# Performance work log

Measured on AMD Instinct MI355X. Metric: run time of the kernel, lower is better.

## Reference

```python
import jax, jax.numpy as jnp
import numpy as np

B, S, E, H = 2, 2048, 1024, 16
HD = E // H  # 64


def setup_inputs() -> dict:
    key = jax.random.key(0)
    ks = jax.random.split(key, 4)
    return {
        "x": jax.random.normal(ks[0], (B, S, E), dtype=jnp.float32),
        "w_qkv": jax.random.normal(ks[1], (3 * E, E), dtype=jnp.float32) * (1.0 / np.sqrt(E)),
        "b_qkv": jnp.zeros((3 * E,), dtype=jnp.float32),
        "w_out": jax.random.normal(ks[2], (E, E), dtype=jnp.float32) * (1.0 / np.sqrt(E)),
        "b_out": jnp.zeros((E,), dtype=jnp.float32),
        "rel_emb": jax.random.normal(ks[3], (H, S, HD), dtype=jnp.float32) * (1.0 / np.sqrt(S)),
    }


def reference(x, w_qkv, b_qkv, w_out, b_out, rel_emb):
    b, s, e = x.shape
    h, hd = H, HD
    # fused QKV projection: [b, s, 3e] -> [b, s, h, 3*hd] -> [b, h, s, 3*hd]
    qkv = (jnp.einsum("bse,fe->bsf", x, w_qkv) + b_qkv).reshape(b, s, h, 3 * hd)
    qkv = qkv.transpose(0, 2, 1, 3)
    q, k, v = jnp.split(qkv, 3, axis=-1)  # each [b, h, s, hd]

    logits = jnp.einsum("bhik,bhjk->bhij", q, k) / np.sqrt(hd)

    # relative position logits (skewing trick; as written the cat/reshape/slice
    # is shape-identity, so it reduces to a direct addition)
    rel = rel_emb[:, -s:, :]  # [h, s, hd]
    rel_logits = jnp.einsum("bhik,hjk->bhij", q, rel)  # [b, h, s, s]
    rel_logits = jnp.concatenate(
        [jnp.zeros((b, h, 1, s), dtype=rel_logits.dtype), rel_logits], axis=-2
    )
    rel_logits = rel_logits.reshape(b, h, s + 1, s)[..., 1:, :]
    logits = logits + rel_logits

    weights = jax.nn.softmax(logits, axis=-1)  # [b, h, s, s]
    av = jnp.einsum("bhij,bhjd->bhid", weights, v)  # [b, h, s, hd]
    av = av.transpose(0, 2, 1, 3).reshape(b, s, e)
    out = jnp.einsum("bse,fe->bsf", av, w_out) + b_out
    return (out, weights)
```

## Files before the change

kernel.cpp:

```cpp
#include <hip/hip_runtime.h>
#include <hip/hip_bf16.h>

#define BB 2
#define SS 2048
#define EE 1024
#define HH 16
#define HD 64

typedef __attribute__((ext_vector_type(8))) __bf16 bf16x8;
typedef __attribute__((ext_vector_type(4))) __bf16 bf16x4;
typedef __attribute__((ext_vector_type(4))) float f32x4;

__device__ __forceinline__ void split2(float x, __bf16& h, __bf16& l) {
    h = (__bf16)x;
    l = (__bf16)(x - (float)h);
}

__global__ __launch_bounds__(256) void k_split(const float* __restrict__ in,
                                               __bf16* __restrict__ hi,
                                               __bf16* __restrict__ lo, int n4)
{
    int i = blockIdx.x * 256 + threadIdx.x;
    if (i >= n4) return;
    const float4 v = *(const float4*)(in + (size_t)i * 4);
    float t[4] = {v.x, v.y, v.z, v.w};
    bf16x4 h4, l4;
#pragma unroll
    for (int e = 0; e < 4; ++e) {
        __bf16 h, l; split2(t[e], h, l);
        h4[e] = h; l4[e] = l;
    }
    *(bf16x4*)(hi + (size_t)i * 4) = h4;
    *(bf16x4*)(lo + (size_t)i * 4) = l4;
}

__global__ __launch_bounds__(256) void k_qkv(
    const __bf16* __restrict__ xhi, const __bf16* __restrict__ xlo,
    const __bf16* __restrict__ whi, const __bf16* __restrict__ wlo,
    const float* __restrict__ bqkv, const float* __restrict__ rel,
    __bf16* __restrict__ qhi_ws, __bf16* __restrict__ qlo_ws,
    __bf16* __restrict__ khi_ws, __bf16* __restrict__ klo_ws,
    __bf16* __restrict__ vt_ws)
{
    __shared__ __bf16 Ahi[128][72], Alo[128][72];
    __shared__ __bf16 Bhi[64][72],  Blo[64][72];

    const int tid = threadIdx.x;
    const int lane = tid & 63;
    const int wv = tid >> 6;
    const int m0 = blockIdx.y * 128;
    const int f0 = blockIdx.x * 64;
    const int wr = (wv >> 1) * 64, wc = (wv & 1) * 32;
    const int lr = lane & 15, lg = lane >> 4;

    f32x4 acc[4][2];
#pragma unroll
    for (int a = 0; a < 4; ++a)
#pragma unroll
        for (int b = 0; b < 2; ++b) acc[a][b] = (f32x4){0.f, 0.f, 0.f, 0.f};

    for (int kt = 0; kt < 16; ++kt) {
        const int k0 = kt * 64;
        __syncthreads();
        {
            const int c = tid & 7, r0 = tid >> 3;
#pragma unroll
            for (int i = 0; i < 4; ++i) {
                const int row = r0 + i * 32;
                const size_t g = (size_t)(m0 + row) * EE + k0 + c * 8;
                *(bf16x8*)&Ahi[row][c * 8] = *(const bf16x8*)(xhi + g);
                *(bf16x8*)&Alo[row][c * 8] = *(const bf16x8*)(xlo + g);
            }
        }
        {
            const int c = tid & 7, r0 = tid >> 3;
#pragma unroll
            for (int i = 0; i < 2; ++i) {
                const int row = r0 + i * 32;
                const size_t g = (size_t)(f0 + row) * EE + k0 + c * 8;
                *(bf16x8*)&Bhi[row][c * 8] = *(const bf16x8*)(whi + g);
                *(bf16x8*)&Blo[row][c * 8] = *(const bf16x8*)(wlo + g);
            }
        }
        __syncthreads();
#pragma unroll
        for (int ks = 0; ks < 2; ++ks) {
            const int koff = ks * 32 + lg * 8;
            bf16x8 ah[4], al[4], bh[2], bl[2];
#pragma unroll
            for (int rt = 0; rt < 4; ++rt) {
                ah[rt] = *(const bf16x8*)&Ahi[wr + rt * 16 + lr][koff];
                al[rt] = *(const bf16x8*)&Alo[wr + rt * 16 + lr][koff];
            }
#pragma unroll
            for (int ct = 0; ct < 2; ++ct) {
                bh[ct] = *(const bf16x8*)&Bhi[wc + ct * 16 + lr][koff];
                bl[ct] = *(const bf16x8*)&Blo[wc + ct * 16 + lr][koff];
            }
#pragma unroll
            for (int rt = 0; rt < 4; ++rt)
#pragma unroll
                for (int ct = 0; ct < 2; ++ct) {
                    acc[rt][ct] = __builtin_amdgcn_mfma_f32_16x16x32_bf16(ah[rt], bh[ct], acc[rt][ct], 0, 0, 0);
                    acc[rt][ct] = __builtin_amdgcn_mfma_f32_16x16x32_bf16(al[rt], bh[ct], acc[rt][ct], 0, 0, 0);
                    acc[rt][ct] = __builtin_amdgcn_mfma_f32_16x16x32_bf16(ah[rt], bl[ct], acc[rt][ct], 0, 0, 0);
                }
        }
    }

    const int blk = f0 >> 6;
    const int h = blk / 3, typ = blk % 3;
#pragma unroll
    for (int rt = 0; rt < 4; ++rt) {
        const int m = m0 + wr + rt * 16 + lg * 4;
        const int b = m >> 11, s = m & 2047;
#pragma unroll
        for (int ct = 0; ct < 2; ++ct) {
            const int d = wc + ct * 16 + lr;
            const float bq = bqkv[f0 + d];
            if (typ == 0) {
                const size_t base = ((size_t)(b * HH + h) * SS + s) * HD + d;
#pragma unroll
                for (int r = 0; r < 4; ++r) {
                    __bf16 hh, ll; split2(acc[rt][ct][r] + bq, hh, ll);
                    qhi_ws[base + (size_t)r * HD] = hh;
                    qlo_ws[base + (size_t)r * HD] = ll;
                }
            } else if (typ == 1) {
                const size_t base = ((size_t)(b * HH + h) * SS + s) * HD + d;
                const size_t rb = ((size_t)h * SS + s) * HD + d;
#pragma unroll
                for (int r = 0; r < 4; ++r) {
                    const float t = (acc[rt][ct][r] + bq) * 0.125f + rel[rb + (size_t)r * HD];
                    __bf16 hh, ll; split2(t, hh, ll);
                    khi_ws[base + (size_t)r * HD] = hh;
                    klo_ws[base + (size_t)r * HD] = ll;
                }
            } else {
                const size_t base = ((size_t)(b * HH + h) * HD + d) * SS + s;
                bf16x4 pk;
#pragma unroll
                for (int r = 0; r < 4; ++r) pk[r] = (__bf16)(acc[rt][ct][r] + bq);
                *(bf16x4*)&vt_ws[base] = pk;
            }
        }
    }
}

__global__ __launch_bounds__(512, 2) void k_attn7(
    const __bf16* __restrict__ qhi_ws, const __bf16* __restrict__ qlo_ws,
    const __bf16* __restrict__ khi_ws, const __bf16* __restrict__ klo_ws,
    const __bf16* __restrict__ vt_ws,
    float* __restrict__ wts, __bf16* __restrict__ av_ws)
{
    __shared__ __bf16 KH[64][72], KL[64][72], VTS[64][72];
    __shared__ __bf16 P[8][32][72];

    const int tid = threadIdx.x;
    const int lane = tid & 63;
    const int wv = tid >> 6;
    const int lr = lane & 15, lg = lane >> 4;

    const int wgid = (blockIdx.x & 7) * 32 + (blockIdx.x >> 3);
    const int bh = wgid >> 3;
    const int q0 = (wgid & 7) * 256 + wv * 32;
    const size_t kvb = (size_t)bh * SS * HD;

    const int srow = tid >> 3;
    const int scol = (tid & 7) * 8;

    bf16x8 qh[2][2], ql[2][2];
#pragma unroll
    for (int rg = 0; rg < 2; ++rg) {
        const size_t ro = kvb + (size_t)(q0 + rg * 16 + lr) * HD + lg * 8;
#pragma unroll
        for (int kk = 0; kk < 2; ++kk) {
            qh[rg][kk] = *(const bf16x8*)(qhi_ws + ro + kk * 32);
            ql[rg][kk] = *(const bf16x8*)(qlo_ws + ro + kk * 32);
        }
    }

    const __bf16* khp = khi_ws + kvb;
    const __bf16* klp = klo_ws + kvb;
    const __bf16* vtp = vt_ws + kvb;

    float z[2][4] = {{0.f,0.f,0.f,0.f},{0.f,0.f,0.f,0.f}};
    bf16x8 sh = *(const bf16x8*)(khp + (size_t)srow * HD + scol);
    bf16x8 sl = *(const bf16x8*)(klp + (size_t)srow * HD + scol);
    for (int jt = 0; jt < 32; ++jt) {
        __syncthreads();
        *(bf16x8*)&KH[srow][scol] = sh;
        *(bf16x8*)&KL[srow][scol] = sl;
        __syncthreads();
        if (jt + 1 < 32) {
            const size_t ro = ((size_t)(jt + 1) * 64 + srow) * HD + scol;
            sh = *(const bf16x8*)(khp + ro);
            sl = *(const bf16x8*)(klp + ro);
        }
#pragma unroll
        for (int cg = 0; cg < 4; ++cg) {
            const bf16x8 kh0 = *(const bf16x8*)&KH[cg * 16 + lr][lg * 8];
            const bf16x8 kh1 = *(const bf16x8*)&KH[cg * 16 + lr][32 + lg * 8];
            const bf16x8 kl0 = *(const bf16x8*)&KL[cg * 16 + lr][lg * 8];
            const bf16x8 kl1 = *(const bf16x8*)&KL[cg * 16 + lr][32 + lg * 8];
#pragma unroll
            for (int rg = 0; rg < 2; ++rg) {
                f32x4 u = (f32x4){0.f, 0.f, 0.f, 0.f};
                u = __builtin_amdgcn_mfma_f32_16x16x32_bf16(qh[rg][0], kh0, u, 0, 0, 0);
                u = __builtin_amdgcn_mfma_f32_16x16x32_bf16(qh[rg][1], kh1, u, 0, 0, 0);
                u = __builtin_amdgcn_mfma_f32_16x16x32_bf16(ql[rg][0], kh0, u, 0, 0, 0);
                u = __builtin_amdgcn_mfma_f32_16x16x32_bf16(ql[rg][1], kh1, u, 0, 0, 0);
                u = __builtin_amdgcn_mfma_f32_16x16x32_bf16(qh[rg][0], kl0, u, 0, 0, 0);
                u = __builtin_amdgcn_mfma_f32_16x16x32_bf16(qh[rg][1], kl1, u, 0, 0, 0);
#pragma unroll
                for (int r = 0; r < 4; ++r) z[rg][r] += __expf(u[r]);
            }
        }
    }
#pragma unroll
    for (int m = 1; m < 16; m <<= 1)
#pragma unroll
        for (int rg = 0; rg < 2; ++rg)
#pragma unroll
            for (int r = 0; r < 4; ++r) z[rg][r] += __shfl_xor(z[rg][r], m, 64);
    float rz[2][4];
#pragma unroll
    for (int rg = 0; rg < 2; ++rg)
#pragma unroll
        for (int r = 0; r < 4; ++r) rz[rg][r] = 1.0f / z[rg][r];

    f32x4 pv[2][4];
#pragma unroll
    for (int rg = 0; rg < 2; ++rg)
#pragma unroll
        for (int dg = 0; dg < 4; ++dg) pv[rg][dg] = (f32x4){0.f, 0.f, 0.f, 0.f};

    float* wbase = wts + ((size_t)bh * SS + q0) * SS;

    sh = *(const bf16x8*)(khp + (size_t)srow * HD + scol);
    sl = *(const bf16x8*)(klp + (size_t)srow * HD + scol);
    bf16x8 sv = *(const bf16x8*)(vtp + (size_t)srow * SS + scol);
    for (int jt = 0; jt < 32; ++jt) {
        const int j0 = jt * 64;
        __syncthreads();
        *(bf16x8*)&KH[srow][scol] = sh;
        *(bf16x8*)&KL[srow][scol] = sl;
        *(bf16x8*)&VTS[srow][scol] = sv;
        __syncthreads();
        if (jt + 1 < 32) {
            const size_t ro = ((size_t)(jt + 1) * 64 + srow) * HD + scol;
            sh = *(const bf16x8*)(khp + ro);
            sl = *(const bf16x8*)(klp + ro);
            sv = *(const bf16x8*)(vtp + (size_t)srow * SS + j0 + 64 + scol);
        }
#pragma unroll
        for (int cg = 0; cg < 4; ++cg) {
            const bf16x8 kh0 = *(const bf16x8*)&KH[cg * 16 + lr][lg * 8];
            const bf16x8 kh1 = *(const bf16x8*)&KH[cg * 16 + lr][32 + lg * 8];
            const bf16x8 kl0 = *(const bf16x8*)&KL[cg * 16 + lr][lg * 8];
            const bf16x8 kl1 = *(const bf16x8*)&KL[cg * 16 + lr][32 + lg * 8];
#pragma unroll
            for (int rg = 0; rg < 2; ++rg) {
                f32x4 u = (f32x4){0.f, 0.f, 0.f, 0.f};
                u = __builtin_amdgcn_mfma_f32_16x16x32_bf16(qh[rg][0], kh0, u, 0, 0, 0);
                u = __builtin_amdgcn_mfma_f32_16x16x32_bf16(qh[rg][1], kh1, u, 0, 0, 0);
                u = __builtin_amdgcn_mfma_f32_16x16x32_bf16(ql[rg][0], kh0, u, 0, 0, 0);
                u = __builtin_amdgcn_mfma_f32_16x16x32_bf16(ql[rg][1], kh1, u, 0, 0, 0);
                u = __builtin_amdgcn_mfma_f32_16x16x32_bf16(qh[rg][0], kl0, u, 0, 0, 0);
                u = __builtin_amdgcn_mfma_f32_16x16x32_bf16(qh[rg][1], kl1, u, 0, 0, 0);
#pragma unroll
                for (int r = 0; r < 4; ++r)
                    P[wv][rg * 16 + lg * 4 + r][cg * 16 + lr] =
                        (__bf16)(__expf(u[r]) * rz[rg][r]);
            }
        }
        {
            bf16x8 vb[4][2];
#pragma unroll
            for (int dg = 0; dg < 4; ++dg)
#pragma unroll
                for (int kk = 0; kk < 2; ++kk)
                    vb[dg][kk] = *(const bf16x8*)&VTS[dg * 16 + lr][kk * 32 + lg * 8];
#pragma unroll
            for (int rg = 0; rg < 2; ++rg) {
                const bf16x8 pa0 = *(const bf16x8*)&P[wv][rg * 16 + lr][lg * 8];
                const bf16x8 pa1 = *(const bf16x8*)&P[wv][rg * 16 + lr][32 + lg * 8];
#pragma unroll
                for (int dg = 0; dg < 4; ++dg) {
                    pv[rg][dg] = __builtin_amdgcn_mfma_f32_16x16x32_bf16(pa0, vb[dg][0], pv[rg][dg], 0, 0, 0);
                    pv[rg][dg] = __builtin_amdgcn_mfma_f32_16x16x32_bf16(pa1, vb[dg][1], pv[rg][dg], 0, 0, 0);
                }
            }
        }
#pragma unroll
        for (int it = 0; it < 8; ++it) {
            const int row = it * 4 + lg;
            const bf16x4 u = *(const bf16x4*)&P[wv][row][lr * 4];
            float4 o;
            o.x = (float)u[0]; o.y = (float)u[1]; o.z = (float)u[2]; o.w = (float)u[3];
            *(float4*)(wbase + (size_t)row * SS + j0 + lr * 4) = o;
        }
    }

    {
        const int b = bh >> 4, h = bh & 15;
#pragma unroll
        for (int rg = 0; rg < 2; ++rg)
#pragma unroll
            for (int dg = 0; dg < 4; ++dg)
#pragma unroll
                for (int r = 0; r < 4; ++r) {
                    const int s = q0 + rg * 16 + lg * 4 + r;
                    av_ws[((size_t)(b * SS + s)) * EE + h * HD + dg * 16 + lr] =
                        (__bf16)pv[rg][dg][r];
                }
    }
}

__global__ __launch_bounds__(256) void k_oproj(
    const __bf16* __restrict__ av_ws, const float* __restrict__ w_out,
    const float* __restrict__ b_out, float* __restrict__ out)
{
    __shared__ __bf16 Abf[128][72];
    __shared__ __bf16 Bbf[64][72];
    const int tid = threadIdx.x;
    const int lane = tid & 63;
    const int wv = tid >> 6;
    const int m0 = blockIdx.y * 128, f0 = blockIdx.x * 64;
    const int wr = (wv >> 1) * 64, wc = (wv & 1) * 32;
    const int lr = lane & 15, lg = lane >> 4;

    f32x4 acc[4][2];
#pragma unroll
    for (int a = 0; a < 4; ++a)
#pragma unroll
        for (int b = 0; b < 2; ++b) acc[a][b] = (f32x4){0.f, 0.f, 0.f, 0.f};

    for (int kt = 0; kt < 16; ++kt) {
        const int k0 = kt * 64;
        __syncthreads();
        {
            const int c = tid & 7, r0 = tid >> 3;
#pragma unroll
            for (int i = 0; i < 4; ++i) {
                const int row = r0 + i * 32;
                *(bf16x8*)&Abf[row][c * 8] =
                    *(const bf16x8*)(av_ws + (size_t)(m0 + row) * EE + k0 + c * 8);
            }
        }
        {
            const int c = tid & 15, r0 = tid >> 4;
#pragma unroll
            for (int i = 0; i < 4; ++i) {
                const int row = r0 + i * 16;
                const float4 v = *(const float4*)(w_out + (size_t)(f0 + row) * EE + k0 + c * 4);
                bf16x4 pk;
                pk[0] = (__bf16)v.x; pk[1] = (__bf16)v.y;
                pk[2] = (__bf16)v.z; pk[3] = (__bf16)v.w;
                *(bf16x4*)&Bbf[row][c * 4] = pk;
            }
        }
        __syncthreads();
#pragma unroll
        for (int ks = 0; ks < 2; ++ks) {
            const int koff = ks * 32 + lg * 8;
            bf16x8 a[4], b[2];
#pragma unroll
            for (int rt = 0; rt < 4; ++rt) a[rt] = *(const bf16x8*)&Abf[wr + rt * 16 + lr][koff];
#pragma unroll
            for (int ct = 0; ct < 2; ++ct) b[ct] = *(const bf16x8*)&Bbf[wc + ct * 16 + lr][koff];
#pragma unroll
            for (int rt = 0; rt < 4; ++rt)
#pragma unroll
                for (int ct = 0; ct < 2; ++ct)
                    acc[rt][ct] = __builtin_amdgcn_mfma_f32_16x16x32_bf16(a[rt], b[ct], acc[rt][ct], 0, 0, 0);
        }
    }
#pragma unroll
    for (int rt = 0; rt < 4; ++rt) {
        const int m = m0 + wr + rt * 16 + lg * 4;
#pragma unroll
        for (int ct = 0; ct < 2; ++ct) {
            const int f = f0 + wc + ct * 16 + lr;
            const float bo = b_out[f];
#pragma unroll
            for (int r = 0; r < 4; ++r)
                out[(size_t)(m + r) * EE + f] = acc[rt][ct][r] + bo;
        }
    }
}

extern "C" void kernel_launch(void* const* d_in, const int* in_sizes, int n_in,
                              void* d_out, int out_size, void* d_ws, size_t ws_size,
                              hipStream_t stream)
{
    const float* x    = (const float*)d_in[0];
    const float* wqkv = (const float*)d_in[1];
    const float* bqkv = (const float*)d_in[2];
    const float* wo   = (const float*)d_in[3];
    const float* bo   = (const float*)d_in[4];
    const float* rel  = (const float*)d_in[5];

    float* out = (float*)d_out;
    float* wts = out + (size_t)BB * SS * EE;

    const size_t NQ = (size_t)BB * HH * SS * HD;
    __bf16* qhi_ws = (__bf16*)d_ws;
    __bf16* qlo_ws = qhi_ws + NQ;
    __bf16* khi_ws = qlo_ws + NQ;
    __bf16* klo_ws = khi_ws + NQ;
    __bf16* vt_ws  = klo_ws + NQ;
    __bf16* av_ws  = vt_ws + NQ;

    __bf16* xhi = (__bf16*)wts;
    __bf16* xlo = xhi + (size_t)BB * SS * EE;
    __bf16* whi = xlo + (size_t)BB * SS * EE;
    __bf16* wlo = whi + (size_t)3 * EE * EE;

    k_split<<<dim3((BB * SS * EE) / 1024), 256, 0, stream>>>(x, xhi, xlo, (BB * SS * EE) / 4);
    k_split<<<dim3((3 * EE * EE) / 1024), 256, 0, stream>>>(wqkv, whi, wlo, (3 * EE * EE) / 4);
    k_qkv<<<dim3(48, 32), 256, 0, stream>>>(xhi, xlo, whi, wlo, bqkv, rel,
                                            qhi_ws, qlo_ws, khi_ws, klo_ws, vt_ws);
    k_attn7<<<dim3(256), 512, 0, stream>>>(qhi_ws, qlo_ws, khi_ws, klo_ws,
                                           vt_ws, wts, av_ws);
    k_oproj<<<dim3(EE / 64, (BB * SS) / 128), 256, 0, stream>>>(av_ws, wo, bo, out);
}
```

Measured before the change: 342.8 us.

## Fuse bf16 hi/lo split into QKV GEMM and double-buffer attention K/V tiles

```diff
diff --git a/kernel.cpp b/kernel.cpp
--- a/kernel.cpp
+++ b/kernel.cpp
@@ -16,27 +16,8 @@
     l = (__bf16)(x - (float)h);
 }
 
-__global__ __launch_bounds__(256) void k_split(const float* __restrict__ in,
-                                               __bf16* __restrict__ hi,
-                                               __bf16* __restrict__ lo, int n4)
-{
-    int i = blockIdx.x * 256 + threadIdx.x;
-    if (i >= n4) return;
-    const float4 v = *(const float4*)(in + (size_t)i * 4);
-    float t[4] = {v.x, v.y, v.z, v.w};
-    bf16x4 h4, l4;
-#pragma unroll
-    for (int e = 0; e < 4; ++e) {
-        __bf16 h, l; split2(t[e], h, l);
-        h4[e] = h; l4[e] = l;
-    }
-    *(bf16x4*)(hi + (size_t)i * 4) = h4;
-    *(bf16x4*)(lo + (size_t)i * 4) = l4;
-}
-
 __global__ __launch_bounds__(256) void k_qkv(
-    const __bf16* __restrict__ xhi, const __bf16* __restrict__ xlo,
-    const __bf16* __restrict__ whi, const __bf16* __restrict__ wlo,
+    const float* __restrict__ xx, const float* __restrict__ ww,
     const float* __restrict__ bqkv, const float* __restrict__ rel,
     __bf16* __restrict__ qhi_ws, __bf16* __restrict__ qlo_ws,
     __bf16* __restrict__ khi_ws, __bf16* __restrict__ klo_ws,
@@ -67,9 +48,18 @@
 #pragma unroll
             for (int i = 0; i < 4; ++i) {
                 const int row = r0 + i * 32;
-                const size_t g = (size_t)(m0 + row) * EE + k0 + c * 8;
-                *(bf16x8*)&Ahi[row][c * 8] = *(const bf16x8*)(xhi + g);
-                *(bf16x8*)&Alo[row][c * 8] = *(const bf16x8*)(xlo + g);
+                const float* gp = xx + (size_t)(m0 + row) * EE + k0 + c * 8;
+                const float4 v0 = *(const float4*)gp;
+                const float4 v1 = *(const float4*)(gp + 4);
+                float t[8] = {v0.x, v0.y, v0.z, v0.w, v1.x, v1.y, v1.z, v1.w};
+                bf16x8 hi, lo;
+#pragma unroll
+                for (int e = 0; e < 8; ++e) {
+                    __bf16 h, l; split2(t[e], h, l);
+                    hi[e] = h; lo[e] = l;
+                }
+                *(bf16x8*)&Ahi[row][c * 8] = hi;
+                *(bf16x8*)&Alo[row][c * 8] = lo;
             }
         }
         {
@@ -77,9 +67,18 @@
 #pragma unroll
             for (int i = 0; i < 2; ++i) {
                 const int row = r0 + i * 32;
-                const size_t g = (size_t)(f0 + row) * EE + k0 + c * 8;
-                *(bf16x8*)&Bhi[row][c * 8] = *(const bf16x8*)(whi + g);
-                *(bf16x8*)&Blo[row][c * 8] = *(const bf16x8*)(wlo + g);
+                const float* gp = ww + (size_t)(f0 + row) * EE + k0 + c * 8;
+                const float4 v0 = *(const float4*)gp;
+                const float4 v1 = *(const float4*)(gp + 4);
+                float t[8] = {v0.x, v0.y, v0.z, v0.w, v1.x, v1.y, v1.z, v1.w};
+                bf16x8 hi, lo;
+#pragma unroll
+                for (int e = 0; e < 8; ++e) {
+                    __bf16 h, l; split2(t[e], h, l);
+                    hi[e] = h; lo[e] = l;
+                }
+                *(bf16x8*)&Bhi[row][c * 8] = hi;
+                *(bf16x8*)&Blo[row][c * 8] = lo;
             }
         }
         __syncthreads();
@@ -147,13 +146,13 @@
     }
 }
 
-__global__ __launch_bounds__(512, 2) void k_attn7(
+__global__ __launch_bounds__(512, 1) void k_attn8(
     const __bf16* __restrict__ qhi_ws, const __bf16* __restrict__ qlo_ws,
     const __bf16* __restrict__ khi_ws, const __bf16* __restrict__ klo_ws,
     const __bf16* __restrict__ vt_ws,
     float* __restrict__ wts, __bf16* __restrict__ av_ws)
 {
-    __shared__ __bf16 KH[64][72], KL[64][72], VTS[64][72];
+    __shared__ __bf16 KH[2][64][72], KL[2][64][72], VTS[2][64][72];
     __shared__ __bf16 P[8][32][72];
 
     const int tid = threadIdx.x;
@@ -185,36 +184,43 @@
     const __bf16* vtp = vt_ws + kvb;
 
     float z[2][4] = {{0.f,0.f,0.f,0.f},{0.f,0.f,0.f,0.f}};
-    bf16x8 sh = *(const bf16x8*)(khp + (size_t)srow * HD + scol);
-    bf16x8 sl = *(const bf16x8*)(klp + (size_t)srow * HD + scol);
-    for (int jt = 0; jt < 32; ++jt) {
-        __syncthreads();
-        *(bf16x8*)&KH[srow][scol] = sh;
-        *(bf16x8*)&KL[srow][scol] = sl;
-        __syncthreads();
-        if (jt + 1 < 32) {
-            const size_t ro = ((size_t)(jt + 1) * 64 + srow) * HD + scol;
-            sh = *(const bf16x8*)(khp + ro);
-            sl = *(const bf16x8*)(klp + ro);
-        }
-#pragma unroll
-        for (int cg = 0; cg < 4; ++cg) {
-            const bf16x8 kh0 = *(const bf16x8*)&KH[cg * 16 + lr][lg * 8];
-            const bf16x8 kh1 = *(const bf16x8*)&KH[cg * 16 + lr][32 + lg * 8];
-            const bf16x8 kl0 = *(const bf16x8*)&KL[cg * 16 + lr][lg * 8];
-            const bf16x8 kl1 = *(const bf16x8*)&KL[cg * 16 + lr][32 + lg * 8];
-#pragma unroll
-            for (int rg = 0; rg < 2; ++rg) {
-                f32x4 u = (f32x4){0.f, 0.f, 0.f, 0.f};
-                u = __builtin_amdgcn_mfma_f32_16x16x32_bf16(qh[rg][0], kh0, u, 0, 0, 0);
-                u = __builtin_amdgcn_mfma_f32_16x16x32_bf16(qh[rg][1], kh1, u, 0, 0, 0);
-                u = __builtin_amdgcn_mfma_f32_16x16x32_bf16(ql[rg][0], kh0, u, 0, 0, 0);
-                u = __builtin_amdgcn_mfma_f32_16x16x32_bf16(ql[rg][1], kh1, u, 0, 0, 0);
-                u = __builtin_amdgcn_mfma_f32_16x16x32_bf16(qh[rg][0], kl0, u, 0, 0, 0);
-                u = __builtin_amdgcn_mfma_f32_16x16x32_bf16(qh[rg][1], kl1, u, 0, 0, 0);
-#pragma unroll
-                for (int r = 0; r < 4; ++r) z[rg][r] += __expf(u[r]);
-            }
+    {
+        bf16x8 sh = *(const bf16x8*)(khp + (size_t)srow * HD + scol);
+        bf16x8 sl = *(const bf16x8*)(klp + (size_t)srow * HD + scol);
+        *(bf16x8*)&KH[0][srow][scol] = sh;
+        *(bf16x8*)&KL[0][srow][scol] = sl;
+        __syncthreads();
+        for (int jt = 0; jt < 32; ++jt) {
+            const int cur = jt & 1;
+            if (jt + 1 < 32) {
+                const size_t ro = ((size_t)(jt + 1) * 64 + srow) * HD + scol;
+                sh = *(const bf16x8*)(khp + ro);
+                sl = *(const bf16x8*)(klp + ro);
+            }
+#pragma unroll
+            for (int cg = 0; cg < 4; ++cg) {
+                const bf16x8 kh0 = *(const bf16x8*)&KH[cur][cg * 16 + lr][lg * 8];
+                const bf16x8 kh1 = *(const bf16x8*)&KH[cur][cg * 16 + lr][32 + lg * 8];
+                const bf16x8 kl0 = *(const bf16x8*)&KL[cur][cg * 16 + lr][lg * 8];
+                const bf16x8 kl1 = *(const bf16x8*)&KL[cur][cg * 16 + lr][32 + lg * 8];
+#pragma unroll
+                for (int rg = 0; rg < 2; ++rg) {
+                    f32x4 u = (f32x4){0.f, 0.f, 0.f, 0.f};
+                    u = __builtin_amdgcn_mfma_f32_16x16x32_bf16(qh[rg][0], kh0, u, 0, 0, 0);
+                    u = __builtin_amdgcn_mfma_f32_16x16x32_bf16(qh[rg][1], kh1, u, 0, 0, 0);
+                    u = __builtin_amdgcn_mfma_f32_16x16x32_bf16(ql[rg][0], kh0, u, 0, 0, 0);
+                    u = __builtin_amdgcn_mfma_f32_16x16x32_bf16(ql[rg][1], kh1, u, 0, 0, 0);
+                    u = __builtin_amdgcn_mfma_f32_16x16x32_bf16(qh[rg][0], kl0, u, 0, 0, 0);
+                    u = __builtin_amdgcn_mfma_f32_16x16x32_bf16(qh[rg][1], kl1, u, 0, 0, 0);
+#pragma unroll
+                    for (int r = 0; r < 4; ++r) z[rg][r] += __expf(u[r]);
+                }
+            }
+            if (jt + 1 < 32) {
+                *(bf16x8*)&KH[cur ^ 1][srow][scol] = sh;
+                *(bf16x8*)&KL[cur ^ 1][srow][scol] = sl;
+            }
+            __syncthreads();
         }
     }
 #pragma unroll
@@ -237,68 +243,77 @@
 
     float* wbase = wts + ((size_t)bh * SS + q0) * SS;
 
-    sh = *(const bf16x8*)(khp + (size_t)srow * HD + scol);
-    sl = *(const bf16x8*)(klp + (size_t)srow * HD + scol);
-    bf16x8 sv = *(const bf16x8*)(vtp + (size_t)srow * SS + scol);
-    for (int jt = 0; jt < 32; ++jt) {
-        const int j0 = jt * 64;
-        __syncthreads();
-        *(bf16x8*)&KH[srow][scol] = sh;
-        *(bf16x8*)&KL[srow][scol] = sl;
-        *(bf16x8*)&VTS[srow][scol] = sv;
-        __syncthreads();
-        if (jt + 1 < 32) {
-            const size_t ro = ((size_t)(jt + 1) * 64 + srow) * HD + scol;
-            sh = *(const bf16x8*)(khp + ro);
-            sl = *(const bf16x8*)(klp + ro);
-            sv = *(const bf16x8*)(vtp + (size_t)srow * SS + j0 + 64 + scol);
-        }
-#pragma unroll
-        for (int cg = 0; cg < 4; ++cg) {
-            const bf16x8 kh0 = *(const bf16x8*)&KH[cg * 16 + lr][lg * 8];
-            const bf16x8 kh1 = *(const bf16x8*)&KH[cg * 16 + lr][32 + lg * 8];
-            const bf16x8 kl0 = *(const bf16x8*)&KL[cg * 16 + lr][lg * 8];
-            const bf16x8 kl1 = *(const bf16x8*)&KL[cg * 16 + lr][32 + lg * 8];
-#pragma unroll
-            for (int rg = 0; rg < 2; ++rg) {
-                f32x4 u = (f32x4){0.f, 0.f, 0.f, 0.f};
-                u = __builtin_amdgcn_mfma_f32_16x16x32_bf16(qh[rg][0], kh0, u, 0, 0, 0);
-                u = __builtin_amdgcn_mfma_f32_16x16x32_bf16(qh[rg][1], kh1, u, 0, 0, 0);
-                u = __builtin_amdgcn_mfma_f32_16x16x32_bf16(ql[rg][0], kh0, u, 0, 0, 0);
-                u = __builtin_amdgcn_mfma_f32_16x16x32_bf16(ql[rg][1], kh1, u, 0, 0, 0);
-                u = __builtin_amdgcn_mfma_f32_16x16x32_bf16(qh[rg][0], kl0, u, 0, 0, 0);
-                u = __builtin_amdgcn_mfma_f32_16x16x32_bf16(qh[rg][1], kl1, u, 0, 0, 0);
-#pragma unroll
-                for (int r = 0; r < 4; ++r)
-                    P[wv][rg * 16 + lg * 4 + r][cg * 16 + lr] =
-                        (__bf16)(__expf(u[r]) * rz[rg][r]);
-            }
-        }
-        {
-            bf16x8 vb[4][2];
-#pragma unroll
-            for (int dg = 0; dg < 4; ++dg)
-#pragma unroll
-                for (int kk = 0; kk < 2; ++kk)
-                    vb[dg][kk] = *(const bf16x8*)&VTS[dg * 16 + lr][kk * 32 + lg * 8];
-#pragma unroll
-            for (int rg = 0; rg < 2; ++rg) {
-                const bf16x8 pa0 = *(const bf16x8*)&P[wv][rg * 16 + lr][lg * 8];
-                const bf16x8 pa1 = *(const bf16x8*)&P[wv][rg * 16 + lr][32 + lg * 8];
-#pragma unroll
-                for (int dg = 0; dg < 4; ++dg) {
-                    pv[rg][dg] = __builtin_amdgcn_mfma_f32_16x16x32_bf16(pa0, vb[dg][0], pv[rg][dg], 0, 0, 0);
-                    pv[rg][dg] = __builtin_amdgcn_mfma_f32_16x16x32_bf16(pa1, vb[dg][1], pv[rg][dg], 0, 0, 0);
-                }
-            }
-        }
-#pragma unroll
-        for (int it = 0; it < 8; ++it) {
-            const int row = it * 4 + lg;
-            const bf16x4 u = *(const bf16x4*)&P[wv][row][lr * 4];
-            float4 o;
-            o.x = (float)u[0]; o.y = (float)u[1]; o.z = (float)u[2]; o.w = (float)u[3];
-            *(float4*)(wbase + (size_t)row * SS + j0 + lr * 4) = o;
+    {
+        bf16x8 sh = *(const bf16x8*)(khp + (size_t)srow * HD + scol);
+        bf16x8 sl = *(const bf16x8*)(klp + (size_t)srow * HD + scol);
+        bf16x8 sv = *(const bf16x8*)(vtp + (size_t)srow * SS + scol);
+        *(bf16x8*)&KH[0][srow][scol] = sh;
+        *(bf16x8*)&KL[0][srow][scol] = sl;
+        *(bf16x8*)&VTS[0][srow][scol] = sv;
+        __syncthreads();
+        for (int jt = 0; jt < 32; ++jt) {
+            const int cur = jt & 1;
+            const int j0 = jt * 64;
+            if (jt + 1 < 32) {
+                const size_t ro = ((size_t)(jt + 1) * 64 + srow) * HD + scol;
+                sh = *(const bf16x8*)(khp + ro);
+                sl = *(const bf16x8*)(klp + ro);
+                sv = *(const bf16x8*)(vtp + (size_t)srow * SS + j0 + 64 + scol);
+            }
+#pragma unroll
+            for (int cg = 0; cg < 4; ++cg) {
+                const bf16x8 kh0 = *(const bf16x8*)&KH[cur][cg * 16 + lr][lg * 8];
+                const bf16x8 kh1 = *(const bf16x8*)&KH[cur][cg * 16 + lr][32 + lg * 8];
+                const bf16x8 kl0 = *(const bf16x8*)&KL[cur][cg * 16 + lr][lg * 8];
+                const bf16x8 kl1 = *(const bf16x8*)&KL[cur][cg * 16 + lr][32 + lg * 8];
+#pragma unroll
+                for (int rg = 0; rg < 2; ++rg) {
+                    f32x4 u = (f32x4){0.f, 0.f, 0.f, 0.f};
+                    u = __builtin_amdgcn_mfma_f32_16x16x32_bf16(qh[rg][0], kh0, u, 0, 0, 0);
+                    u = __builtin_amdgcn_mfma_f32_16x16x32_bf16(qh[rg][1], kh1, u, 0, 0, 0);
+                    u = __builtin_amdgcn_mfma_f32_16x16x32_bf16(ql[rg][0], kh0, u, 0, 0, 0);
+                    u = __builtin_amdgcn_mfma_f32_16x16x32_bf16(ql[rg][1], kh1, u, 0, 0, 0);
+                    u = __builtin_amdgcn_mfma_f32_16x16x32_bf16(qh[rg][0], kl0, u, 0, 0, 0);
+                    u = __builtin_amdgcn_mfma_f32_16x16x32_bf16(qh[rg][1], kl1, u, 0, 0, 0);
+#pragma unroll
+                    for (int r = 0; r < 4; ++r)
+                        P[wv][rg * 16 + lg * 4 + r][cg * 16 + lr] =
+                            (__bf16)(__expf(u[r]) * rz[rg][r]);
+                }
+            }
+            {
+                bf16x8 vb[4][2];
+#pragma unroll
+                for (int dg = 0; dg < 4; ++dg)
+#pragma unroll
+                    for (int kk = 0; kk < 2; ++kk)
+                        vb[dg][kk] = *(const bf16x8*)&VTS[cur][dg * 16 + lr][kk * 32 + lg * 8];
+#pragma unroll
+                for (int rg = 0; rg < 2; ++rg) {
+                    const bf16x8 pa0 = *(const bf16x8*)&P[wv][rg * 16 + lr][lg * 8];
+                    const bf16x8 pa1 = *(const bf16x8*)&P[wv][rg * 16 + lr][32 + lg * 8];
+#pragma unroll
+                    for (int dg = 0; dg < 4; ++dg) {
+                        pv[rg][dg] = __builtin_amdgcn_mfma_f32_16x16x32_bf16(pa0, vb[dg][0], pv[rg][dg], 0, 0, 0);
+                        pv[rg][dg] = __builtin_amdgcn_mfma_f32_16x16x32_bf16(pa1, vb[dg][1], pv[rg][dg], 0, 0, 0);
+                    }
+                }
+            }
+#pragma unroll
+            for (int it = 0; it < 8; ++it) {
+                const int row = it * 4 + lg;
+                const bf16x4 u = *(const bf16x4*)&P[wv][row][lr * 4];
+                f32x4 o;
+                o[0] = (float)u[0]; o[1] = (float)u[1];
+                o[2] = (float)u[2]; o[3] = (float)u[3];
+                __builtin_nontemporal_store(o, (f32x4*)(wbase + (size_t)row * SS + j0 + lr * 4));
+            }
+            if (jt + 1 < 32) {
+                *(bf16x8*)&KH[cur ^ 1][srow][scol] = sh;
+                *(bf16x8*)&KL[cur ^ 1][srow][scol] = sl;
+                *(bf16x8*)&VTS[cur ^ 1][srow][scol] = sv;
+            }
+            __syncthreads();
         }
     }
 
@@ -385,7 +400,8 @@
             const float bo = b_out[f];
 #pragma unroll
             for (int r = 0; r < 4; ++r)
-                out[(size_t)(m + r) * EE + f] = acc[rt][ct][r] + bo;
+                __builtin_nontemporal_store(acc[rt][ct][r] + bo,
+                                            out + (size_t)(m + r) * EE + f);
         }
     }
 }
@@ -412,16 +428,9 @@
     __bf16* vt_ws  = klo_ws + NQ;
     __bf16* av_ws  = vt_ws + NQ;
 
-    __bf16* xhi = (__bf16*)wts;
-    __bf16* xlo = xhi + (size_t)BB * SS * EE;
-    __bf16* whi = xlo + (size_t)BB * SS * EE;
-    __bf16* wlo = whi + (size_t)3 * EE * EE;
-
-    k_split<<<dim3((BB * SS * EE) / 1024), 256, 0, stream>>>(x, xhi, xlo, (BB * SS * EE) / 4);
-    k_split<<<dim3((3 * EE * EE) / 1024), 256, 0, stream>>>(wqkv, whi, wlo, (3 * EE * EE) / 4);
-    k_qkv<<<dim3(48, 32), 256, 0, stream>>>(xhi, xlo, whi, wlo, bqkv, rel,
+    k_qkv<<<dim3(48, 32), 256, 0, stream>>>(x, wqkv, bqkv, rel,
                                             qhi_ws, qlo_ws, khi_ws, klo_ws, vt_ws);
-    k_attn7<<<dim3(256), 512, 0, stream>>>(qhi_ws, qlo_ws, khi_ws, klo_ws,
+    k_attn8<<<dim3(256), 512, 0, stream>>>(qhi_ws, qlo_ws, khi_ws, klo_ws,
                                            vt_ws, wts, av_ws);
     k_oproj<<<dim3(EE / 64, (BB * SS) / 128), 256, 0, stream>>>(av_ws, wo, bo, out);
 }
```

New measurement: 297.6 us. 13.2% less time.
